# Optimization experiments

Measured on AMD Instinct MI355X. Metric: run time of the kernel, lower is better.

## Reference

```python
import jax, jax.numpy as jnp
import numpy as np

DIM = 1024
NUM_HEADS = 16


def setup_inputs() -> dict:
    key = jax.random.key(0)
    ks = jax.random.split(key, 8)
    B, N, C = 2, 2048, DIM
    x = jax.random.normal(ks[0], (B, N, C), dtype=jnp.float32)
    attn_mask = jnp.zeros((B, 1, N, N), dtype=jnp.float32)
    # learned parameters
    w_qkv = jax.random.normal(ks[1], (3 * C, C), dtype=jnp.float32) * (C ** -0.5)
    q_bias = jnp.zeros((C,), dtype=jnp.float32)
    k_bias = jnp.zeros((C,), dtype=jnp.float32)
    v_bias = jnp.zeros((C,), dtype=jnp.float32)
    w_proj = jax.random.normal(ks[2], (C, C), dtype=jnp.float32) * (C ** -0.5)
    b_proj = jnp.zeros((C,), dtype=jnp.float32)
    return {
        "x": x, "attn_mask": attn_mask,
        "w_qkv": w_qkv, "q_bias": q_bias, "k_bias": k_bias, "v_bias": v_bias,
        "w_proj": w_proj, "b_proj": b_proj,
        "num_heads": NUM_HEADS,
    }


def reference(x, attn_mask, w_qkv, q_bias, k_bias, v_bias, w_proj, b_proj, num_heads):
    B, N, C = x.shape
    H = num_heads
    hd = C // H
    scale = hd ** -0.5
    alpha = 32.0
    # fused qkv projection with concatenated biases
    qkv_bias = jnp.concatenate([q_bias, k_bias, v_bias])
    qkv = x @ w_qkv.T + qkv_bias                       # [B, N, 3C]
    qkv = qkv.reshape(B, N, 3, H, hd).transpose(2, 0, 3, 1, 4)  # [3, B, H, N, hd]
    q, k, v = qkv[0], qkv[1], qkv[2]
    # stabilization trick: scale q down by alpha, compute scores, re-scale after max-subtraction
    q = q * (scale / alpha)
    attn = jnp.einsum('bhld,bhmd->bhlm', q, k)         # [B, H, N, N]
    attn = (attn - jnp.max(attn, axis=-1, keepdims=True)) * alpha
    attn = attn + attn_mask                            # additive mask, broadcast over heads
    attn = jax.nn.softmax(attn, axis=-1)
    out = jnp.einsum('bhlm,bhmd->blhd', attn, v).reshape(B, N, C)
    out = out @ w_proj.T + b_proj
    return out
```

## Files before the change

### kernel.cpp

```cpp
#include <hip/hip_runtime.h>

typedef unsigned short u16;
typedef __bf16   bf16x8 __attribute__((ext_vector_type(8)));
typedef float    f32x4  __attribute__((ext_vector_type(4)));
typedef unsigned u32x4v __attribute__((ext_vector_type(4)));
typedef u16      u16x8  __attribute__((ext_vector_type(8)));

#define DEV __device__ __forceinline__

DEV u16 tobf(float f) {
  return __builtin_bit_cast(unsigned short, (__bf16)f);
}

DEV unsigned pack2(float a, float b) {
  return (unsigned)tobf(a) | ((unsigned)tobf(b) << 16);
}

DEV f32x4 fzero() { f32x4 z; z[0]=0.f; z[1]=0.f; z[2]=0.f; z[3]=0.f; return z; }

DEV void async_cp16(void* lds, const void* g) {
  __builtin_amdgcn_global_load_lds(
      (const __attribute__((address_space(1))) void*)g,
      (__attribute__((address_space(3))) void*)lds, 16, 0, 0);
}

DEV void cvt8(const float* __restrict__ in, u16* __restrict__ out, int i) {
  const float4* in4 = (const float4*)in;
  float4 a = in4[2*i], b = in4[2*i+1];
  u16x8 r;
  r[0]=tobf(a.x); r[1]=tobf(a.y); r[2]=tobf(a.z); r[3]=tobf(a.w);
  r[4]=tobf(b.x); r[5]=tobf(b.y); r[6]=tobf(b.z); r[7]=tobf(b.w);
  *(u16x8*)(out + 8*(size_t)i) = r;
}

__global__ void k_zero_flag(unsigned* f) {
  if (threadIdx.x == 0 && blockIdx.x == 0) *f = 0u;
}

__global__ __launch_bounds__(256)
void k_pre(const float* __restrict__ x, const float* __restrict__ wqkv,
           const float* __restrict__ wproj,
           u16* __restrict__ xb, u16* __restrict__ wqkvb, u16* __restrict__ wprojb,
           const u32x4v* __restrict__ mask, unsigned* __restrict__ flag)
{
  const int tid = blockIdx.x * blockDim.x + threadIdx.x;
  const int stride = gridDim.x * blockDim.x;
  for (int i = tid; i < 524288; i += stride) cvt8(x, xb, i);
  for (int i = tid; i < 393216; i += stride) cvt8(wqkv, wqkvb, i);
  for (int i = tid; i < 131072; i += stride) cvt8(wproj, wprojb, i);
  unsigned o = 0;
  for (int i = tid; i < 2097152; i += stride) {
    u32x4v v = mask[i];
    o |= v[0] | v[1] | v[2] | v[3];
  }
  if (o & 0x7fffffffu) atomicOr(flag, 1u);
}

template<int EPI>
__global__ __launch_bounds__(256)
void k_gemm_nt(const u16* __restrict__ A, const u16* __restrict__ B,
               int N, int K, int nbn,
               const float* __restrict__ bq, const float* __restrict__ bk,
               const float* __restrict__ bv,
               u16* __restrict__ qo, u16* __restrict__ ko, u16* __restrict__ vto,
               float* __restrict__ fo, const float* __restrict__ bp)
{
  __shared__ u16 sA[2][4096];
  __shared__ u16 sB[2][4096];

  const int tid  = threadIdx.x;
  const int lane = tid & 63;
  const int wave = tid >> 6;
  const int lr = lane & 15, lg = lane >> 4;
  const int wr = wave >> 1, wc = wave & 1;

  const int per = gridDim.x >> 3;
  const int bid = blockIdx.x;
  const int swz = (bid & 7) * per + (bid >> 3);
  const int bm0 = (swz / nbn) << 7;
  const int bn0 = (swz - (swz / nbn) * nbn) << 7;

  const size_t Kb = (size_t)K * 2;

  auto stage = [&](int buf, int kt) {
#pragma unroll
    for (int j = 0; j < 2; ++j) {
      int off = (tid + j * 256) << 4;
      int row = off >> 6;
      int ch  = (off & 63) >> 4;
      int gch = ch ^ (row & 3);
      async_cp16((char*)&sA[buf][0] + off,
                 (const char*)A + (size_t)(bm0 + row) * Kb + (size_t)kt * 64 + gch * 16);
      async_cp16((char*)&sB[buf][0] + off,
                 (const char*)B + (size_t)(bn0 + row) * Kb + (size_t)kt * 64 + gch * 16);
    }
  };

  f32x4 acc[4][4];
#pragma unroll
  for (int i = 0; i < 4; ++i)
#pragma unroll
    for (int j = 0; j < 4; ++j) acc[i][j] = fzero();

  const int nk = K >> 5;
  stage(0, 0);
  __syncthreads();

  for (int kt = 0; kt < nk; ++kt) {
    const int cur = kt & 1;
    if (kt + 1 < nk) stage(cur ^ 1, kt + 1);

    bf16x8 af[4], bfr[4];
#pragma unroll
    for (int mi = 0; mi < 4; ++mi) {
      int row = (wr << 6) + (mi << 4) + lr;
      int addr = (row << 6) + ((lg ^ (row & 3)) << 4);
      af[mi] = *(const bf16x8*)((const char*)&sA[cur][0] + addr);
    }
#pragma unroll
    for (int ni = 0; ni < 4; ++ni) {
      int row = (wc << 6) + (ni << 4) + lr;
      int addr = (row << 6) + ((lg ^ (row & 3)) << 4);
      bfr[ni] = *(const bf16x8*)((const char*)&sB[cur][0] + addr);
    }
#pragma unroll
    for (int mi = 0; mi < 4; ++mi)
#pragma unroll
      for (int ni = 0; ni < 4; ++ni)
        acc[mi][ni] = __builtin_amdgcn_mfma_f32_16x16x32_bf16(af[mi], bfr[ni], acc[mi][ni], 0, 0, 0);

    __syncthreads();
  }

#pragma unroll
  for (int mi = 0; mi < 4; ++mi) {
#pragma unroll
    for (int ni = 0; ni < 4; ++ni) {
      int col = bn0 + (wc << 6) + (ni << 4) + lr;
      if (EPI == 0) {
        int s = col >> 10, hd = col & 1023;
        int h = hd >> 6, d = hd & 63;
        float bias = (s == 0 ? bq[hd] : (s == 1 ? bk[hd] : bv[hd]));
#pragma unroll
        for (int r = 0; r < 4; ++r) {
          int m = bm0 + (wr << 6) + (mi << 4) + (lg << 2) + r;
          int b = m >> 11, n = m & 2047;
          float v = acc[mi][ni][r] + bias;
          if (s == 0) v *= 0.125f;
          u16 val = tobf(v);
          size_t bh = (size_t)(b * 16 + h);
          if (s == 0)      qo[(bh * 2048 + n) * 64 + d] = val;
          else if (s == 1) ko[(bh * 2048 + n) * 64 + d] = val;
          else             vto[(bh * 64 + d) * 2048 + n] = val;
        }
      } else {
        float bias = bp[col];
#pragma unroll
        for (int r = 0; r < 4; ++r) {
          int m = bm0 + (wr << 6) + (mi << 4) + (lg << 2) + r;
          fo[(size_t)m * N + col] = acc[mi][ni][r] + bias;
        }
      }
    }
  }
}

__global__ __launch_bounds__(256)
void k_attn(const u16* __restrict__ qb, const u16* __restrict__ kb,
            const u16* __restrict__ vtb, u16* __restrict__ ao,
            const float* __restrict__ mask, const unsigned* __restrict__ flag)
{
  constexpr int N = 2048, D = 64;
  __shared__ u16 sK[2][4096];
  __shared__ u16 sV[2][4096];

  const int tid  = threadIdx.x;
  const int lane = tid & 63;
  const int wave = tid >> 6;
  const int lr = lane & 15, lg = lane >> 4;

  const int bid  = blockIdx.x;
  const int xcd  = bid & 7, slot = bid >> 3;
  const int bh   = xcd + 8 * (slot >> 5);
  const int qt   = slot & 31;
  const int b    = bh >> 4, h = bh & 15;

  const u16* Kbh = kb  + (size_t)bh * N * D;
  const u16* Vbh = vtb + (size_t)bh * D * N;
  const int q_lo = qt * 64 + wave * 16;
  const int qg   = q_lo + lr;

  bf16x8 qf[2];
  {
    const u16* qrow = qb + ((size_t)bh * N + qg) * D;
    qf[0] = *(const bf16x8*)(qrow + lg * 8);
    qf[1] = *(const bf16x8*)(qrow + 32 + lg * 8);
  }

  const unsigned use_mask = *flag;
  const float* maskb = mask + (size_t)b * N * N;

  float m_run = -INFINITY, lsum = 0.f;
  f32x4 o[4];
#pragma unroll
  for (int i = 0; i < 4; ++i) o[i] = fzero();

  auto stage = [&](int buf, int kt) {
#pragma unroll
    for (int j = 0; j < 2; ++j) {
      int off = (tid + j * 256) << 4;
      int row = off >> 7;
      int ch  = (off & 127) >> 4;
      int gch = ch ^ (row & 7);
      async_cp16((char*)&sK[buf][0] + off,
                 (const char*)Kbh + (size_t)(kt * 64 + row) * 128 + gch * 16);
      async_cp16((char*)&sV[buf][0] + off,
                 (const char*)Vbh + (size_t)row * (N * 2) + (size_t)kt * 128 + gch * 16);
    }
  };

  stage(0, 0);
  __syncthreads();

  const float L2E = 1.44269504088896340736f;

  for (int kt = 0; kt < N / 64; ++kt) {
    const int cur = kt & 1;
    if (kt + 1 < N / 64) stage(cur ^ 1, kt + 1);

    f32x4 sc[4];
#pragma unroll
    for (int mi = 0; mi < 4; ++mi) sc[mi] = fzero();
    __builtin_amdgcn_s_setprio(1);
#pragma unroll
    for (int mi = 0; mi < 4; ++mi)
#pragma unroll
      for (int ks = 0; ks < 2; ++ks) {
        int row = (mi << 4) + lr;
        int addr = (row << 7) + ((((ks << 2) + lg) ^ (row & 7)) << 4);
        bf16x8 kf = *(const bf16x8*)((const char*)&sK[cur][0] + addr);
        sc[mi] = __builtin_amdgcn_mfma_f32_16x16x32_bf16(kf, qf[ks], sc[mi], 0, 0, 0);
      }
    __builtin_amdgcn_s_setprio(0);

    if (use_mask) {
#pragma unroll
      for (int mi = 0; mi < 4; ++mi)
#pragma unroll
        for (int r = 0; r < 4; ++r) {
          int kg = kt * 64 + (mi << 4) + (lg << 2) + r;
          sc[mi][r] += maskb[(size_t)qg * N + kg];
        }
    }

    float a0 = fmaxf(fmaxf(sc[0][0], sc[0][1]), fmaxf(sc[0][2], sc[0][3]));
    float a1 = fmaxf(fmaxf(sc[1][0], sc[1][1]), fmaxf(sc[1][2], sc[1][3]));
    float a2 = fmaxf(fmaxf(sc[2][0], sc[2][1]), fmaxf(sc[2][2], sc[2][3]));
    float a3 = fmaxf(fmaxf(sc[3][0], sc[3][1]), fmaxf(sc[3][2], sc[3][3]));
    float pm = fmaxf(fmaxf(a0, a1), fmaxf(a2, a3));
    pm = fmaxf(pm, __shfl_xor(pm, 16, 64));
    pm = fmaxf(pm, __shfl_xor(pm, 32, 64));

    if (__any(pm > m_run + 8.f)) {
      const float m_new = fmaxf(m_run, pm);
      const float f = __builtin_amdgcn_exp2f((m_run - m_new) * L2E);
      m_run = m_new;
      float fr[4];
#pragma unroll
      for (int r = 0; r < 4; ++r) fr[r] = __shfl(f, (lg << 2) + r, 64);
#pragma unroll
      for (int ni = 0; ni < 4; ++ni)
#pragma unroll
        for (int r = 0; r < 4; ++r) o[ni][r] *= fr[r];
      lsum *= f;
    }

    const float mL2 = m_run * L2E;
    float p[4][4];
    float rs = 0.f;
#pragma unroll
    for (int mi = 0; mi < 4; ++mi)
#pragma unroll
      for (int r = 0; r < 4; ++r) {
        p[mi][r] = __builtin_amdgcn_exp2f(__builtin_fmaf(sc[mi][r], L2E, -mL2));
        rs += p[mi][r];
      }
    rs += __shfl_xor(rs, 16, 64);
    rs += __shfl_xor(rs, 32, 64);
    lsum += rs;

    unsigned P32[4][2];
#pragma unroll
    for (int mi = 0; mi < 4; ++mi)
#pragma unroll
      for (int rp = 0; rp < 2; ++rp)
        P32[mi][rp] = pack2(p[mi][2 * rp], p[mi][2 * rp + 1]);

    bf16x8 pf[2];
#pragma unroll
    for (int ks = 0; ks < 2; ++ks) {
      u32x4v w;
#pragma unroll
      for (int wd = 0; wd < 4; ++wd) {
        int src = lr + ((((lg << 1) + (wd >> 1)) & 3) << 4);
        unsigned vlo = __shfl(P32[2 * ks + 0][wd & 1], src, 64);
        unsigned vhi = __shfl(P32[2 * ks + 1][wd & 1], src, 64);
        w[wd] = (lg & 2) ? vhi : vlo;
      }
      pf[ks] = __builtin_bit_cast(bf16x8, w);
    }

    __builtin_amdgcn_s_setprio(1);
#pragma unroll
    for (int ni = 0; ni < 4; ++ni)
#pragma unroll
      for (int ks = 0; ks < 2; ++ks) {
        int drow = (ni << 4) + lr;
        int addr = (drow << 7) + ((((ks << 2) + lg) ^ (drow & 7)) << 4);
        bf16x8 vf = *(const bf16x8*)((const char*)&sV[cur][0] + addr);
        o[ni] = __builtin_amdgcn_mfma_f32_16x16x32_bf16(pf[ks], vf, o[ni], 0, 0, 0);
      }
    __builtin_amdgcn_s_setprio(0);

    __syncthreads();
  }

  const float inv = 1.0f / lsum;
  float ivr[4];
#pragma unroll
  for (int r = 0; r < 4; ++r) ivr[r] = __shfl(inv, (lg << 2) + r, 64);

#pragma unroll
  for (int ni = 0; ni < 4; ++ni) {
    int d = (ni << 4) + lr;
#pragma unroll
    for (int r = 0; r < 4; ++r) {
      int qrow = q_lo + (lg << 2) + r;
      ao[((size_t)(b * N + qrow)) * 1024 + h * 64 + d] = tobf(o[ni][r] * ivr[r]);
    }
  }
}

extern "C" void kernel_launch(void* const* d_in, const int* in_sizes, int n_in,
                              void* d_out, int out_size, void* d_ws, size_t ws_size,
                              hipStream_t stream) {
  const float* x      = (const float*)d_in[0];
  const float* mask   = (const float*)d_in[1];
  const float* w_qkv  = (const float*)d_in[2];
  const float* q_bias = (const float*)d_in[3];
  const float* k_bias = (const float*)d_in[4];
  const float* v_bias = (const float*)d_in[5];
  const float* w_proj = (const float*)d_in[6];
  const float* b_proj = (const float*)d_in[7];
  float* out = (float*)d_out;

  const int B = 2, N = 2048, C = 1024;
  const int M = B * N;

  u16* ws     = (u16*)d_ws;
  u16* xb     = ws;
  u16* wqkvb  = ws + 4194304;
  u16* wprojb = ws + 7340032;
  u16* qbuf   = ws + 8388608;
  u16* kbuf   = ws + 12582912;
  u16* vtbuf  = ws + 16777216;
  unsigned* flag = (unsigned*)(ws + 20971520);
  u16* aob    = xb;

  k_zero_flag<<<1, 64, 0, stream>>>(flag);
  k_pre<<<2048, 256, 0, stream>>>(x, w_qkv, w_proj, xb, wqkvb, wprojb,
                                  (const u32x4v*)mask, flag);

  k_gemm_nt<0><<<(M / 128) * (3 * C / 128), 256, 0, stream>>>(
      xb, wqkvb, 3 * C, C, 3 * C / 128,
      q_bias, k_bias, v_bias, qbuf, kbuf, vtbuf, nullptr, nullptr);

  k_attn<<<B * 16 * (N / 64), 256, 0, stream>>>(qbuf, kbuf, vtbuf, aob, mask, flag);

  k_gemm_nt<1><<<(M / 128) * (C / 128), 256, 0, stream>>>(
      aob, wprojb, C, C, C / 128,
      nullptr, nullptr, nullptr, nullptr, nullptr, nullptr, out, b_proj);
}
```

Measured before the change: 159.5 us.

## Switch attention kernel to 32x32x16 MFMA with 128-query tiles and permlane swaps

Rewrites the flash-attention inner loop to use 32x32x16 bf16 MFMAs, so each wave handles 32 query rows and each block 128 queries, halving the grid size. The P-matrix relayout between the QK and PV matmuls now uses v_permlane32_swap instead of many cross-lane shuffles. This reuses each K/V LDS tile over twice as many queries and cuts shuffle and reduction overhead. In exchange it raises register pressure and halves the number of blocks, which may lower occupancy and leave fewer blocks to spread across CUs.

```diff
diff --git a/kernel.cpp b/kernel.cpp
--- a/kernel.cpp
+++ b/kernel.cpp
@@ -3,6 +3,7 @@
 typedef unsigned short u16;
 typedef __bf16   bf16x8 __attribute__((ext_vector_type(8)));
 typedef float    f32x4  __attribute__((ext_vector_type(4)));
+typedef float    f32x16 __attribute__((ext_vector_type(16)));
 typedef unsigned u32x4v __attribute__((ext_vector_type(4)));
 typedef u16      u16x8  __attribute__((ext_vector_type(8)));
 
@@ -170,40 +171,42 @@
             const u16* __restrict__ vtb, u16* __restrict__ ao,
             const float* __restrict__ mask, const unsigned* __restrict__ flag)
 {
-  constexpr int N = 2048, D = 64;
+  constexpr int N = 2048;
   __shared__ u16 sK[2][4096];
   __shared__ u16 sV[2][4096];
 
   const int tid  = threadIdx.x;
   const int lane = tid & 63;
   const int wave = tid >> 6;
-  const int lr = lane & 15, lg = lane >> 4;
+  const int l31  = lane & 31;
+  const int hi   = lane >> 5;
 
   const int bid  = blockIdx.x;
   const int xcd  = bid & 7, slot = bid >> 3;
-  const int bh   = xcd + 8 * (slot >> 5);
-  const int qt   = slot & 31;
+  const int bh   = xcd + 8 * (slot >> 4);
+  const int qt   = slot & 15;
   const int b    = bh >> 4, h = bh & 15;
 
-  const u16* Kbh = kb  + (size_t)bh * N * D;
-  const u16* Vbh = vtb + (size_t)bh * D * N;
-  const int q_lo = qt * 64 + wave * 16;
-  const int qg   = q_lo + lr;
-
-  bf16x8 qf[2];
+  const u16* Kbh = kb  + (size_t)bh * N * 64;
+  const u16* Vbh = vtb + (size_t)bh * 64 * N;
+  const int q_lo = qt * 128 + wave * 32;
+  const int qg   = q_lo + l31;
+
+  bf16x8 qf[4];
   {
-    const u16* qrow = qb + ((size_t)bh * N + qg) * D;
-    qf[0] = *(const bf16x8*)(qrow + lg * 8);
-    qf[1] = *(const bf16x8*)(qrow + 32 + lg * 8);
+    const u16* qrow = qb + ((size_t)bh * N + qg) * 64;
+#pragma unroll
+    for (int ks = 0; ks < 4; ++ks)
+      qf[ks] = *(const bf16x8*)(qrow + ks * 16 + hi * 8);
   }
 
   const unsigned use_mask = *flag;
   const float* maskb = mask + (size_t)b * N * N;
 
   float m_run = -INFINITY, lsum = 0.f;
-  f32x4 o[4];
-#pragma unroll
-  for (int i = 0; i < 4; ++i) o[i] = fzero();
+  f32x16 o0, o1;
+#pragma unroll
+  for (int r = 0; r < 16; ++r) { o0[r] = 0.f; o1[r] = 0.f; }
 
   auto stage = [&](int buf, int kt) {
 #pragma unroll
@@ -228,116 +231,125 @@
     const int cur = kt & 1;
     if (kt + 1 < N / 64) stage(cur ^ 1, kt + 1);
 
-    f32x4 sc[4];
-#pragma unroll
-    for (int mi = 0; mi < 4; ++mi) sc[mi] = fzero();
+    f32x16 sc0, sc1;
+#pragma unroll
+    for (int r = 0; r < 16; ++r) { sc0[r] = 0.f; sc1[r] = 0.f; }
+
     __builtin_amdgcn_s_setprio(1);
 #pragma unroll
-    for (int mi = 0; mi < 4; ++mi)
-#pragma unroll
-      for (int ks = 0; ks < 2; ++ks) {
-        int row = (mi << 4) + lr;
-        int addr = (row << 7) + ((((ks << 2) + lg) ^ (row & 7)) << 4);
-        bf16x8 kf = *(const bf16x8*)((const char*)&sK[cur][0] + addr);
-        sc[mi] = __builtin_amdgcn_mfma_f32_16x16x32_bf16(kf, qf[ks], sc[mi], 0, 0, 0);
+    for (int ks = 0; ks < 4; ++ks) {
+      int row0 = l31;
+      int a0 = (row0 << 7) + ((((ks << 1) + hi) ^ (row0 & 7)) << 4);
+      bf16x8 kf0 = *(const bf16x8*)((const char*)&sK[cur][0] + a0);
+      sc0 = __builtin_amdgcn_mfma_f32_32x32x16_bf16(kf0, qf[ks], sc0, 0, 0, 0);
+      int row1 = 32 + l31;
+      int a1 = (row1 << 7) + ((((ks << 1) + hi) ^ (row1 & 7)) << 4);
+      bf16x8 kf1 = *(const bf16x8*)((const char*)&sK[cur][0] + a1);
+      sc1 = __builtin_amdgcn_mfma_f32_32x32x16_bf16(kf1, qf[ks], sc1, 0, 0, 0);
+    }
+    __builtin_amdgcn_s_setprio(0);
+
+    if (use_mask) {
+#pragma unroll
+      for (int r = 0; r < 16; ++r) {
+        int krow = (r & 3) + 8 * (r >> 2) + 4 * hi;
+        sc0[r] += maskb[(size_t)qg * N + kt * 64 + krow];
+        sc1[r] += maskb[(size_t)qg * N + kt * 64 + 32 + krow];
       }
-    __builtin_amdgcn_s_setprio(0);
-
-    if (use_mask) {
-#pragma unroll
-      for (int mi = 0; mi < 4; ++mi)
-#pragma unroll
-        for (int r = 0; r < 4; ++r) {
-          int kg = kt * 64 + (mi << 4) + (lg << 2) + r;
-          sc[mi][r] += maskb[(size_t)qg * N + kg];
-        }
-    }
-
-    float a0 = fmaxf(fmaxf(sc[0][0], sc[0][1]), fmaxf(sc[0][2], sc[0][3]));
-    float a1 = fmaxf(fmaxf(sc[1][0], sc[1][1]), fmaxf(sc[1][2], sc[1][3]));
-    float a2 = fmaxf(fmaxf(sc[2][0], sc[2][1]), fmaxf(sc[2][2], sc[2][3]));
-    float a3 = fmaxf(fmaxf(sc[3][0], sc[3][1]), fmaxf(sc[3][2], sc[3][3]));
-    float pm = fmaxf(fmaxf(a0, a1), fmaxf(a2, a3));
-    pm = fmaxf(pm, __shfl_xor(pm, 16, 64));
+    }
+
+    float t[8];
+#pragma unroll
+    for (int r = 0; r < 8; ++r)
+      t[r] = fmaxf(fmaxf(sc0[r], sc0[r + 8]), fmaxf(sc1[r], sc1[r + 8]));
+#pragma unroll
+    for (int r = 0; r < 4; ++r) t[r] = fmaxf(t[r], t[r + 4]);
+    float pm = fmaxf(fmaxf(t[0], t[1]), fmaxf(t[2], t[3]));
     pm = fmaxf(pm, __shfl_xor(pm, 32, 64));
 
     if (__any(pm > m_run + 8.f)) {
       const float m_new = fmaxf(m_run, pm);
       const float f = __builtin_amdgcn_exp2f((m_run - m_new) * L2E);
       m_run = m_new;
-      float fr[4];
-#pragma unroll
-      for (int r = 0; r < 4; ++r) fr[r] = __shfl(f, (lg << 2) + r, 64);
-#pragma unroll
-      for (int ni = 0; ni < 4; ++ni)
-#pragma unroll
-        for (int r = 0; r < 4; ++r) o[ni][r] *= fr[r];
+      float fr[16];
+#pragma unroll
+      for (int r = 0; r < 16; ++r)
+        fr[r] = __shfl(f, (r & 3) + 8 * (r >> 2) + 4 * hi, 64);
+#pragma unroll
+      for (int r = 0; r < 16; ++r) { o0[r] *= fr[r]; o1[r] *= fr[r]; }
       lsum *= f;
     }
 
     const float mL2 = m_run * L2E;
-    float p[4][4];
-    float rs = 0.f;
-#pragma unroll
-    for (int mi = 0; mi < 4; ++mi)
-#pragma unroll
-      for (int r = 0; r < 4; ++r) {
-        p[mi][r] = __builtin_amdgcn_exp2f(__builtin_fmaf(sc[mi][r], L2E, -mL2));
-        rs += p[mi][r];
-      }
-    rs += __shfl_xor(rs, 16, 64);
+    float rs0 = 0.f, rs1 = 0.f, rs2 = 0.f, rs3 = 0.f;
+#pragma unroll
+    for (int r = 0; r < 16; r += 4) {
+      sc0[r]   = __builtin_amdgcn_exp2f(__builtin_fmaf(sc0[r],   L2E, -mL2));
+      sc0[r+1] = __builtin_amdgcn_exp2f(__builtin_fmaf(sc0[r+1], L2E, -mL2));
+      sc0[r+2] = __builtin_amdgcn_exp2f(__builtin_fmaf(sc0[r+2], L2E, -mL2));
+      sc0[r+3] = __builtin_amdgcn_exp2f(__builtin_fmaf(sc0[r+3], L2E, -mL2));
+      sc1[r]   = __builtin_amdgcn_exp2f(__builtin_fmaf(sc1[r],   L2E, -mL2));
+      sc1[r+1] = __builtin_amdgcn_exp2f(__builtin_fmaf(sc1[r+1], L2E, -mL2));
+      sc1[r+2] = __builtin_amdgcn_exp2f(__builtin_fmaf(sc1[r+2], L2E, -mL2));
+      sc1[r+3] = __builtin_amdgcn_exp2f(__builtin_fmaf(sc1[r+3], L2E, -mL2));
+      rs0 += sc0[r]   + sc1[r];
+      rs1 += sc0[r+1] + sc1[r+1];
+      rs2 += sc0[r+2] + sc1[r+2];
+      rs3 += sc0[r+3] + sc1[r+3];
+    }
+    float rs = (rs0 + rs1) + (rs2 + rs3);
     rs += __shfl_xor(rs, 32, 64);
     lsum += rs;
 
-    unsigned P32[4][2];
-#pragma unroll
-    for (int mi = 0; mi < 4; ++mi)
-#pragma unroll
-      for (int rp = 0; rp < 2; ++rp)
-        P32[mi][rp] = pack2(p[mi][2 * rp], p[mi][2 * rp + 1]);
-
-    bf16x8 pf[2];
-#pragma unroll
-    for (int ks = 0; ks < 2; ++ks) {
-      u32x4v w;
-#pragma unroll
-      for (int wd = 0; wd < 4; ++wd) {
-        int src = lr + ((((lg << 1) + (wd >> 1)) & 3) << 4);
-        unsigned vlo = __shfl(P32[2 * ks + 0][wd & 1], src, 64);
-        unsigned vhi = __shfl(P32[2 * ks + 1][wd & 1], src, 64);
-        w[wd] = (lg & 2) ? vhi : vlo;
-      }
-      pf[ks] = __builtin_bit_cast(bf16x8, w);
+    unsigned P32_0[8], P32_1[8];
+#pragma unroll
+    for (int tt = 0; tt < 8; ++tt) {
+      P32_0[tt] = pack2(sc0[2 * tt], sc0[2 * tt + 1]);
+      P32_1[tt] = pack2(sc1[2 * tt], sc1[2 * tt + 1]);
+    }
+
+    bf16x8 pa[4];
+#pragma unroll
+    for (int ks16 = 0; ks16 < 4; ++ks16) {
+      const int b4 = (ks16 & 1) << 2;
+      unsigned c0, c1, c2, c3;
+      if (ks16 < 2) { c0 = P32_0[b4]; c2 = P32_0[b4+2]; c1 = P32_0[b4+1]; c3 = P32_0[b4+3]; }
+      else          { c0 = P32_1[b4]; c2 = P32_1[b4+2]; c1 = P32_1[b4+1]; c3 = P32_1[b4+3]; }
+      asm volatile("v_permlane32_swap_b32 %0, %1" : "+v"(c0), "+v"(c2));
+      asm volatile("v_permlane32_swap_b32 %0, %1" : "+v"(c1), "+v"(c3));
+      u32x4v w; w[0] = c0; w[1] = c1; w[2] = c2; w[3] = c3;
+      pa[ks16] = __builtin_bit_cast(bf16x8, w);
     }
 
     __builtin_amdgcn_s_setprio(1);
 #pragma unroll
-    for (int ni = 0; ni < 4; ++ni)
-#pragma unroll
-      for (int ks = 0; ks < 2; ++ks) {
-        int drow = (ni << 4) + lr;
-        int addr = (drow << 7) + ((((ks << 2) + lg) ^ (drow & 7)) << 4);
-        bf16x8 vf = *(const bf16x8*)((const char*)&sV[cur][0] + addr);
-        o[ni] = __builtin_amdgcn_mfma_f32_16x16x32_bf16(pf[ks], vf, o[ni], 0, 0, 0);
-      }
+    for (int ks16 = 0; ks16 < 4; ++ks16) {
+      int row0 = l31;
+      int a0 = (row0 << 7) + ((((ks16 << 1) + hi) ^ (row0 & 7)) << 4);
+      bf16x8 vf0 = *(const bf16x8*)((const char*)&sV[cur][0] + a0);
+      o0 = __builtin_amdgcn_mfma_f32_32x32x16_bf16(pa[ks16], vf0, o0, 0, 0, 0);
+      int row1 = 32 + l31;
+      int a1 = (row1 << 7) + ((((ks16 << 1) + hi) ^ (row1 & 7)) << 4);
+      bf16x8 vf1 = *(const bf16x8*)((const char*)&sV[cur][0] + a1);
+      o1 = __builtin_amdgcn_mfma_f32_32x32x16_bf16(pa[ks16], vf1, o1, 0, 0, 0);
+    }
     __builtin_amdgcn_s_setprio(0);
 
     __syncthreads();
   }
 
   const float inv = 1.0f / lsum;
-  float ivr[4];
-#pragma unroll
-  for (int r = 0; r < 4; ++r) ivr[r] = __shfl(inv, (lg << 2) + r, 64);
-
-#pragma unroll
-  for (int ni = 0; ni < 4; ++ni) {
-    int d = (ni << 4) + lr;
-#pragma unroll
-    for (int r = 0; r < 4; ++r) {
-      int qrow = q_lo + (lg << 2) + r;
-      ao[((size_t)(b * N + qrow)) * 1024 + h * 64 + d] = tobf(o[ni][r] * ivr[r]);
-    }
+  float ivr[16];
+#pragma unroll
+  for (int r = 0; r < 16; ++r)
+    ivr[r] = __shfl(inv, (r & 3) + 8 * (r >> 2) + 4 * hi, 64);
+
+#pragma unroll
+  for (int r = 0; r < 16; ++r) {
+    int qrow = q_lo + (r & 3) + 8 * (r >> 2) + 4 * hi;
+    size_t base = ((size_t)(b * N + qrow)) * 1024 + h * 64;
+    ao[base + l31]      = tobf(o0[r] * ivr[r]);
+    ao[base + 32 + l31] = tobf(o1[r] * ivr[r]);
   }
 }
 
@@ -375,7 +387,7 @@
       xb, wqkvb, 3 * C, C, 3 * C / 128,
       q_bias, k_bias, v_bias, qbuf, kbuf, vtbuf, nullptr, nullptr);
 
-  k_attn<<<B * 16 * (N / 64), 256, 0, stream>>>(qbuf, kbuf, vtbuf, aob, mask, flag);
+  k_attn<<<B * 16 * (N / 128), 256, 0, stream>>>(qbuf, kbuf, vtbuf, aob, mask, flag);
 
   k_gemm_nt<1><<<(M / 128) * (C / 128), 256, 0, stream>>>(
       aob, wprojb, C, C, C / 128,
```

After: 143.1 us. 10.3% less time.
